# Optimization experiments

Measured on AMD Instinct MI355X. Metric: run time of the kernel, lower is better.

The kernel has to match this reference:

```python
import jax, jax.numpy as jnp
import numpy as np

D_HEAD = 64
KERNEL = 7


def make_neighbourhood_mask(kernel: int, ch: int, cw: int) -> jnp.ndarray:
    """Boolean mask [ch*cw, ch*cw]; True where key is inside the query's k x k window."""
    h_ramp = jnp.arange(ch)
    w_ramp = jnp.arange(cw)
    h_pos, w_pos = jnp.meshgrid(h_ramp, w_ramp, indexing='ij')  # [ch, cw]
    start_h = jnp.clip(h_pos - kernel // 2, 0, ch - kernel)[..., None, None]
    end_h = start_h + kernel
    start_w = jnp.clip(w_pos - kernel // 2, 0, cw - kernel)[..., None, None]
    end_w = start_w + kernel
    h_range = h_ramp.reshape(1, 1, ch, 1)
    w_range = w_ramp.reshape(1, 1, 1, cw)
    mask = (h_range >= start_h) & (h_range < end_h) & (w_range >= start_w) & (w_range < end_w)
    return mask.reshape(ch * cw, ch * cw)


def setup_inputs() -> dict:
    key = jax.random.key(0)
    k1, k2, k3 = jax.random.split(key, 3)
    B, H, W, D = 2, 64, 64, 384
    x = jax.random.normal(k1, (B, H, W, D), dtype=jnp.float32)
    w_qkv = jax.random.normal(k2, (3 * D, D), dtype=jnp.float32) * 0.02
    w_out = jax.random.normal(k3, (D, D), dtype=jnp.float32) * 0.02
    return {"x": x, "w_qkv": w_qkv, "w_out": w_out}


def reference(x, w_qkv, w_out):
    B, H, W, D = x.shape
    nh = D // D_HEAD
    N = H * W
    # qkv projection: Linear(D, 3D, bias=False) -> x @ w_qkv.T
    qkv = jnp.einsum('bhwd,ed->bhwe', x, w_qkv)  # [B,H,W,3D]
    # 'n h w (t nh e) -> t n nh (h w) e'
    qkv = qkv.reshape(B, N, 3, nh, D_HEAD)
    qkv = jnp.transpose(qkv, (2, 0, 3, 1, 4))  # [3, B, nh, N, e]
    q, k, v = qkv[0], qkv[1], qkv[2]
    mask = make_neighbourhood_mask(KERNEL, H, W)  # [N, N] bool
    scale = 1.0 / jnp.sqrt(jnp.asarray(D_HEAD, dtype=x.dtype))
    scores = jnp.einsum('bnqe,bnke->bnqk', q, k) * scale  # [B,nh,N,N]
    neg = jnp.asarray(jnp.finfo(scores.dtype).min, dtype=scores.dtype)
    scores = jnp.where(mask[None, None], scores, neg)
    attn = jax.nn.softmax(scores, axis=-1)
    out = jnp.einsum('bnqk,bnke->bnqe', attn, v)  # [B,nh,N,e]
    # 'n nh (h w) e -> n h w (nh e)'
    out = jnp.transpose(out, (0, 2, 1, 3)).reshape(B, H, W, D)
    return jnp.einsum('bhwd,ed->bhwe', out, w_out)
```

## Files before the change

### kernel.cpp

```cpp
#include <hip/hip_runtime.h>
#include <hip/hip_bf16.h>

typedef __attribute__((ext_vector_type(8))) short bf16x8;
typedef __attribute__((ext_vector_type(4))) short s16x4;
typedef __attribute__((ext_vector_type(4))) float fx4;

#define MFMA16(a, b, c) __builtin_amdgcn_mfma_f32_16x16x32_bf16((a), (b), (c), 0, 0, 0)

__device__ __forceinline__ short f2bf(float f) {
  unsigned u = __float_as_uint(f);
  u += 0x7fffu + ((u >> 16) & 1u);
  return (short)(u >> 16);
}

__device__ __forceinline__ void gl_lds16(const short* g, short* l) {
  __builtin_amdgcn_global_load_lds((const __attribute__((address_space(1))) void*)(g),
                                   (__attribute__((address_space(3))) void*)(l), 16, 0, 0);
}

__global__ __launch_bounds__(256) void convert_k(
    const float* __restrict__ x, const float* __restrict__ wq, const float* __restrict__ wo,
    short* __restrict__ xb, short* __restrict__ wb, short* __restrict__ wob) {
  const int i4 = (blockIdx.x * 256 + threadIdx.x) * 4;
  {
    float4 v = *(const float4*)(x + i4);
    s16x4 s; s[0] = f2bf(v.x); s[1] = f2bf(v.y); s[2] = f2bf(v.z); s[3] = f2bf(v.w);
    *(s16x4*)(xb + i4) = s;
  }
  if (i4 < 1152 * 384) {
    float4 v = *(const float4*)(wq + i4);
    s16x4 s; s[0] = f2bf(v.x); s[1] = f2bf(v.y); s[2] = f2bf(v.z); s[3] = f2bf(v.w);
    *(s16x4*)(wb + i4) = s;
  }
  if (i4 < 384 * 384) {
    float4 v = *(const float4*)(wo + i4);
    s16x4 s; s[0] = f2bf(v.x); s[1] = f2bf(v.y); s[2] = f2bf(v.z); s[3] = f2bf(v.w);
    *(s16x4*)(wob + i4) = s;
  }
}

__global__ __launch_bounds__(256) void qkv_gemm(
    const short* __restrict__ A, const short* __restrict__ Bw,
    short* __restrict__ qb, short* __restrict__ kb, short* __restrict__ vb) {
  __shared__ __align__(16) short As[128 * 64];
  __shared__ __align__(16) short Bs[128 * 64];
  const int orig = (blockIdx.x & 7) * 72 + (blockIdx.x >> 3);
  const int mt = orig / 9, nt = orig % 9;
  const int m0 = mt * 128, n0 = nt * 128;
  const int tid = threadIdx.x;
  const int lane = tid & 63, w = tid >> 6;
  const int wr = w >> 1, wc = w & 1;
  const int l15 = lane & 15, l4 = lane >> 4;
  const int srow = lane >> 3;
  const int scol = ((lane & 7) ^ (srow & 7)) * 8;
  const fx4 vzero = {0.f, 0.f, 0.f, 0.f};
  fx4 acc[4][4];
#pragma unroll
  for (int i = 0; i < 4; i++)
#pragma unroll
    for (int j = 0; j < 4; j++) acc[i][j] = vzero;

  for (int kt = 0; kt < 384; kt += 64) {
    __syncthreads();
#pragma unroll
    for (int q = 0; q < 4; q++) {
      gl_lds16(A  + (size_t)(m0 + w * 32 + q * 8 + srow) * 384 + kt + scol, As + (w * 32 + q * 8) * 64);
      gl_lds16(Bw + (size_t)(n0 + w * 32 + q * 8 + srow) * 384 + kt + scol, Bs + (w * 32 + q * 8) * 64);
    }
    __syncthreads();
    bf16x8 af[4][2], bfr[4][2];
#pragma unroll
    for (int i = 0; i < 4; i++) {
      const int ra = wr * 64 + i * 16 + l15;
      const int rb = wc * 64 + i * 16 + l15;
#pragma unroll
      for (int kk = 0; kk < 2; kk++) {
        af[i][kk]  = *(const bf16x8*)(As + ra * 64 + (((kk * 4 + l4) ^ (ra & 7)) * 8));
        bfr[i][kk] = *(const bf16x8*)(Bs + rb * 64 + (((kk * 4 + l4) ^ (rb & 7)) * 8));
      }
    }
#pragma unroll
    for (int i = 0; i < 4; i++)
#pragma unroll
      for (int j = 0; j < 4; j++) {
        acc[i][j] = MFMA16(af[i][0], bfr[j][0], acc[i][j]);
        acc[i][j] = MFMA16(af[i][1], bfr[j][1], acc[i][j]);
      }
  }
#pragma unroll
  for (int j = 0; j < 4; j++) {
    const int e = n0 + wc * 64 + j * 16 + l15;
    const int t = e / 384;
    const int rem = e - t * 384;
    const int head = rem >> 6, d = rem & 63;
    short* __restrict__ dst = (t == 0) ? qb : (t == 1) ? kb : vb;
#pragma unroll
    for (int i = 0; i < 4; i++) {
      const int mb = m0 + wr * 64 + i * 16 + l4 * 4;
#pragma unroll
      for (int r = 0; r < 4; r++) {
        const int m = mb + r;
        const int b = m >> 12, pix = m & 4095;
        dst[((b * 6 + head) * 4096 + pix) * 64 + d] = f2bf(acc[i][j][r]);
      }
    }
  }
}

__global__ __launch_bounds__(256) void natt_k(
    const short* __restrict__ qg, const short* __restrict__ kg, const short* __restrict__ vg,
    short* __restrict__ ob) {
  __shared__ __align__(16) short lds[30976];
  short* Ks = lds;
  short* Vt = lds + 16128;
  short* Ps = lds;

  const int bid = (blockIdx.x & 7) * 96 + (blockIdx.x >> 3);
  const int tile = bid & 63, bh = bid >> 6;
  const int h0 = (tile >> 3) * 8, w0 = (tile & 7) * 8;
  const int ph0 = max(h0 - 3, 0), pw0 = max(w0 - 3, 0);
  const int prows = min(h0 + 4, 57) + 7 - ph0;
  const int pcols = min(w0 + 4, 57) + 7 - pw0;
  const short* kb = kg + (size_t)bh * 4096 * 64;
  const short* vb = vg + (size_t)bh * 4096 * 64;
  const short* qb = qg + (size_t)bh * 4096 * 64;
  const int tid = threadIdx.x;

  for (int i = tid; i < 224 * 8; i += 256) {
    const int kk = i >> 3, dc = i & 7;
    const int kr = kk >> 4, kc = kk & 15;
    const int krc = min(kr, prows - 1), kcc = min(kc, pcols - 1);
    const int pix = (ph0 + krc) * 64 + (pw0 + kcc);
    *(bf16x8*)(Ks + kk * 72 + dc * 8) = *(const bf16x8*)(kb + pix * 64 + dc * 8);
  }
  if (tid < 224) {
    const int kk = tid;
    const int kr = kk >> 4, kc = kk & 15;
    const int krc = min(kr, prows - 1), kcc = min(kc, pcols - 1);
    const int pix = (ph0 + krc) * 64 + (pw0 + kcc);
#pragma unroll
    for (int dc = 0; dc < 8; dc++) {
      const bf16x8 vv = *(const bf16x8*)(vb + pix * 64 + dc * 8);
#pragma unroll
      for (int j = 0; j < 8; j++) Vt[(dc * 8 + j) * 232 + kk] = vv[j];
    }
  }
  __syncthreads();

  const int lane = tid & 63, w = tid >> 6;
  const int l15 = lane & 15, l4 = lane >> 4;

  const int qa = w * 16 + l15;
  const int qpixa = (h0 + (qa >> 3)) * 64 + (w0 + (qa & 7));
  const bf16x8 aq0 = *(const bf16x8*)(qb + qpixa * 64 + l4 * 8);
  const bf16x8 aq1 = *(const bf16x8*)(qb + qpixa * 64 + 32 + l4 * 8);

  const fx4 vzero = {0.f, 0.f, 0.f, 0.f};
  fx4 s[14];
#pragma unroll
  for (int n = 0; n < 14; n++) s[n] = vzero;
#pragma unroll
  for (int n = 0; n < 14; n++) {
    const bf16x8 b0 = *(const bf16x8*)(Ks + (n * 16 + l15) * 72 + l4 * 8);
    const bf16x8 b1 = *(const bf16x8*)(Ks + (n * 16 + l15) * 72 + 32 + l4 * 8);
    s[n] = MFMA16(aq0, b0, s[n]);
    s[n] = MFMA16(aq1, b1, s[n]);
  }

#pragma unroll
  for (int r = 0; r < 4; r++) {
    const int q = w * 16 + l4 * 4 + r;
    const int qh = h0 + (q >> 3), qw = w0 + (q & 7);
    const int sh = min(max(qh - 3, 0), 57) - ph0;
    const int sw = min(max(qw - 3, 0), 57) - pw0;
    float m = -1e30f;
#pragma unroll
    for (int n = 0; n < 14; n++) {
      const bool valid = (n >= sh) && (n < sh + 7) && (l15 >= sw) && (l15 < sw + 7);
      const float val = valid ? s[n][r] * 0.125f : -1e30f;
      s[n][r] = val;
      m = fmaxf(m, val);
    }
    m = fmaxf(m, __shfl_xor(m, 1));
    m = fmaxf(m, __shfl_xor(m, 2));
    m = fmaxf(m, __shfl_xor(m, 4));
    m = fmaxf(m, __shfl_xor(m, 8));
    float sum = 0.f;
#pragma unroll
    for (int n = 0; n < 14; n++) {
      const float e = __expf(s[n][r] - m);
      s[n][r] = e;
      sum += e;
    }
    sum += __shfl_xor(sum, 1);
    sum += __shfl_xor(sum, 2);
    sum += __shfl_xor(sum, 4);
    sum += __shfl_xor(sum, 8);
    const float inv = 1.f / sum;
#pragma unroll
    for (int n = 0; n < 14; n++) s[n][r] *= inv;
  }

  __syncthreads();

#pragma unroll
  for (int n = 0; n < 14; n++)
#pragma unroll
    for (int r = 0; r < 4; r++)
      Ps[(w * 16 + l4 * 4 + r) * 232 + n * 16 + l15] = f2bf(s[n][r]);

  __syncthreads();

  fx4 o[4];
#pragma unroll
  for (int j = 0; j < 4; j++) o[j] = vzero;
#pragma unroll
  for (int ks = 0; ks < 7; ks++) {
    const bf16x8 pa = *(const bf16x8*)(Ps + (w * 16 + l15) * 232 + ks * 32 + l4 * 8);
#pragma unroll
    for (int j = 0; j < 4; j++) {
      const bf16x8 vf = *(const bf16x8*)(Vt + (j * 16 + l15) * 232 + ks * 32 + l4 * 8);
      o[j] = MFMA16(pa, vf, o[j]);
    }
  }

  const int b = bh / 6, head = bh % 6;
#pragma unroll
  for (int j = 0; j < 4; j++) {
    const int d = j * 16 + l15;
#pragma unroll
    for (int r = 0; r < 4; r++) {
      const int q = w * 16 + l4 * 4 + r;
      const int pix = (h0 + (q >> 3)) * 64 + (w0 + (q & 7));
      ob[(size_t)(b * 4096 + pix) * 384 + head * 64 + d] = f2bf(o[j][r]);
    }
  }
}

__global__ __launch_bounds__(256) void out_gemm(
    const short* __restrict__ A, const short* __restrict__ Bw, float* __restrict__ out) {
  __shared__ __align__(16) short As[64 * 64];
  __shared__ __align__(16) short Bs[128 * 64];
  const int orig = (blockIdx.x & 7) * 48 + (blockIdx.x >> 3);
  const int mt = orig / 3, nt = orig % 3;
  const int m0 = mt * 64, n0 = nt * 128;
  const int tid = threadIdx.x;
  const int lane = tid & 63, w = tid >> 6;
  const int wr = w >> 1, wc = w & 1;
  const int l15 = lane & 15, l4 = lane >> 4;
  const int srow = lane >> 3;
  const int scol = ((lane & 7) ^ (srow & 7)) * 8;
  const fx4 vzero = {0.f, 0.f, 0.f, 0.f};
  fx4 acc[2][4];
#pragma unroll
  for (int i = 0; i < 2; i++)
#pragma unroll
    for (int j = 0; j < 4; j++) acc[i][j] = vzero;

  for (int kt = 0; kt < 384; kt += 64) {
    __syncthreads();
#pragma unroll
    for (int q = 0; q < 2; q++)
      gl_lds16(A + (size_t)(m0 + w * 16 + q * 8 + srow) * 384 + kt + scol, As + (w * 16 + q * 8) * 64);
#pragma unroll
    for (int q = 0; q < 4; q++)
      gl_lds16(Bw + (size_t)(n0 + w * 32 + q * 8 + srow) * 384 + kt + scol, Bs + (w * 32 + q * 8) * 64);
    __syncthreads();
    bf16x8 af[2][2], bfr[4][2];
#pragma unroll
    for (int i = 0; i < 2; i++) {
      const int ra = wr * 32 + i * 16 + l15;
#pragma unroll
      for (int kk = 0; kk < 2; kk++)
        af[i][kk] = *(const bf16x8*)(As + ra * 64 + (((kk * 4 + l4) ^ (ra & 7)) * 8));
    }
#pragma unroll
    for (int j = 0; j < 4; j++) {
      const int rb = wc * 64 + j * 16 + l15;
#pragma unroll
      for (int kk = 0; kk < 2; kk++)
        bfr[j][kk] = *(const bf16x8*)(Bs + rb * 64 + (((kk * 4 + l4) ^ (rb & 7)) * 8));
    }
#pragma unroll
    for (int i = 0; i < 2; i++)
#pragma unroll
      for (int j = 0; j < 4; j++) {
        acc[i][j] = MFMA16(af[i][0], bfr[j][0], acc[i][j]);
        acc[i][j] = MFMA16(af[i][1], bfr[j][1], acc[i][j]);
      }
  }
#pragma unroll
  for (int j = 0; j < 4; j++) {
    const int e = n0 + wc * 64 + j * 16 + l15;
#pragma unroll
    for (int i = 0; i < 2; i++) {
      const int mb = m0 + wr * 32 + i * 16 + l4 * 4;
#pragma unroll
      for (int r = 0; r < 4; r++)
        out[(size_t)(mb + r) * 384 + e] = acc[i][j][r];
    }
  }
}

extern "C" void kernel_launch(void* const* d_in, const int* in_sizes, int n_in,
                              void* d_out, int out_size, void* d_ws, size_t ws_size,
                              hipStream_t stream) {
  const float* x  = (const float*)d_in[0];
  const float* wq = (const float*)d_in[1];
  const float* wo = (const float*)d_in[2];
  float* out = (float*)d_out;

  short* xb  = (short*)d_ws;
  short* wb  = xb + 8192 * 384;
  short* wob = wb + 1152 * 384;
  short* qb  = wob + 384 * 384;
  short* kb  = qb + 3145728;
  short* vb  = kb + 3145728;
  short* ob  = vb + 3145728;

  convert_k<<<3072, 256, 0, stream>>>(x, wq, wo, xb, wb, wob);
  qkv_gemm<<<576, 256, 0, stream>>>(xb, wb, qb, kb, vb);
  natt_k<<<768, 256, 0, stream>>>(qb, kb, vb, ob);
  out_gemm<<<384, 256, 0, stream>>>(ob, wob, out);
}
```

Baseline: 51.62 us.

## Fuse fp32-to-bf16 conversion into GEMM loads with register-prefetched double-buffered LDS

Drops the separate conversion kernel. The QKV and output GEMMs now read fp32 inputs and weights directly, convert them to bf16 in registers, and write them into swizzled LDS. Staging is double-buffered, with the next K-tile prefetched into registers while the current tile runs on MFMA, and one barrier per iteration instead of two. This removes a kernel launch and a full round trip of the bf16 copies through memory. In exchange, fp32 global traffic doubles inside the GEMMs, the weights are converted again by every block, and register pressure and LDS use rise.

```diff
diff --git a/kernel.cpp b/kernel.cpp
--- a/kernel.cpp
+++ b/kernel.cpp
@@ -2,7 +2,6 @@
 #include <hip/hip_bf16.h>
 
 typedef __attribute__((ext_vector_type(8))) short bf16x8;
-typedef __attribute__((ext_vector_type(4))) short s16x4;
 typedef __attribute__((ext_vector_type(4))) float fx4;
 
 #define MFMA16(a, b, c) __builtin_amdgcn_mfma_f32_16x16x32_bf16((a), (b), (c), 0, 0, 0)
@@ -13,37 +12,18 @@
   return (short)(u >> 16);
 }
 
-__device__ __forceinline__ void gl_lds16(const short* g, short* l) {
-  __builtin_amdgcn_global_load_lds((const __attribute__((address_space(1))) void*)(g),
-                                   (__attribute__((address_space(3))) void*)(l), 16, 0, 0);
-}
-
-__global__ __launch_bounds__(256) void convert_k(
-    const float* __restrict__ x, const float* __restrict__ wq, const float* __restrict__ wo,
-    short* __restrict__ xb, short* __restrict__ wb, short* __restrict__ wob) {
-  const int i4 = (blockIdx.x * 256 + threadIdx.x) * 4;
-  {
-    float4 v = *(const float4*)(x + i4);
-    s16x4 s; s[0] = f2bf(v.x); s[1] = f2bf(v.y); s[2] = f2bf(v.z); s[3] = f2bf(v.w);
-    *(s16x4*)(xb + i4) = s;
-  }
-  if (i4 < 1152 * 384) {
-    float4 v = *(const float4*)(wq + i4);
-    s16x4 s; s[0] = f2bf(v.x); s[1] = f2bf(v.y); s[2] = f2bf(v.z); s[3] = f2bf(v.w);
-    *(s16x4*)(wb + i4) = s;
-  }
-  if (i4 < 384 * 384) {
-    float4 v = *(const float4*)(wo + i4);
-    s16x4 s; s[0] = f2bf(v.x); s[1] = f2bf(v.y); s[2] = f2bf(v.z); s[3] = f2bf(v.w);
-    *(s16x4*)(wob + i4) = s;
-  }
+__device__ __forceinline__ bf16x8 cvt8(float4 a, float4 b) {
+  bf16x8 r;
+  r[0] = f2bf(a.x); r[1] = f2bf(a.y); r[2] = f2bf(a.z); r[3] = f2bf(a.w);
+  r[4] = f2bf(b.x); r[5] = f2bf(b.y); r[6] = f2bf(b.z); r[7] = f2bf(b.w);
+  return r;
 }
 
 __global__ __launch_bounds__(256) void qkv_gemm(
-    const short* __restrict__ A, const short* __restrict__ Bw,
+    const float* __restrict__ A, const float* __restrict__ Bw,
     short* __restrict__ qb, short* __restrict__ kb, short* __restrict__ vb) {
-  __shared__ __align__(16) short As[128 * 64];
-  __shared__ __align__(16) short Bs[128 * 64];
+  __shared__ __align__(16) short As[2][128 * 64];
+  __shared__ __align__(16) short Bs[2][128 * 64];
   const int orig = (blockIdx.x & 7) * 72 + (blockIdx.x >> 3);
   const int mt = orig / 9, nt = orig % 9;
   const int m0 = mt * 128, n0 = nt * 128;
@@ -51,8 +31,12 @@
   const int lane = tid & 63, w = tid >> 6;
   const int wr = w >> 1, wc = w & 1;
   const int l15 = lane & 15, l4 = lane >> 4;
-  const int srow = lane >> 3;
-  const int scol = ((lane & 7) ^ (srow & 7)) * 8;
+  const int srow = tid >> 1, shalf = tid & 1;
+  const float* ga = A  + (size_t)(m0 + srow) * 384 + shalf * 32;
+  const float* gb = Bw + (size_t)(n0 + srow) * 384 + shalf * 32;
+  const int wbase = srow * 64;
+  const int sw7 = srow & 7;
+
   const fx4 vzero = {0.f, 0.f, 0.f, 0.f};
   fx4 acc[4][4];
 #pragma unroll
@@ -60,23 +44,39 @@
 #pragma unroll
     for (int j = 0; j < 4; j++) acc[i][j] = vzero;
 
-  for (int kt = 0; kt < 384; kt += 64) {
+  float4 ra[8], rb[8];
+#pragma unroll
+  for (int i = 0; i < 8; i++) {
+    ra[i] = *(const float4*)(ga + i * 4);
+    rb[i] = *(const float4*)(gb + i * 4);
+  }
+#pragma unroll
+  for (int c = 0; c < 4; c++) {
+    *(bf16x8*)(&As[0][wbase + (((shalf * 4 + c) ^ sw7) * 8)]) = cvt8(ra[2 * c], ra[2 * c + 1]);
+    *(bf16x8*)(&Bs[0][wbase + (((shalf * 4 + c) ^ sw7) * 8)]) = cvt8(rb[2 * c], rb[2 * c + 1]);
+  }
+
+  int cur = 0;
+  for (int t = 0; t < 6; ++t) {
+    if (t < 5) {
+#pragma unroll
+      for (int i = 0; i < 8; i++) {
+        ra[i] = *(const float4*)(ga + (t + 1) * 64 + i * 4);
+        rb[i] = *(const float4*)(gb + (t + 1) * 64 + i * 4);
+      }
+    }
     __syncthreads();
-#pragma unroll
-    for (int q = 0; q < 4; q++) {
-      gl_lds16(A  + (size_t)(m0 + w * 32 + q * 8 + srow) * 384 + kt + scol, As + (w * 32 + q * 8) * 64);
-      gl_lds16(Bw + (size_t)(n0 + w * 32 + q * 8 + srow) * 384 + kt + scol, Bs + (w * 32 + q * 8) * 64);
-    }
-    __syncthreads();
+    const short* as_c = As[cur];
+    const short* bs_c = Bs[cur];
     bf16x8 af[4][2], bfr[4][2];
 #pragma unroll
     for (int i = 0; i < 4; i++) {
-      const int ra = wr * 64 + i * 16 + l15;
-      const int rb = wc * 64 + i * 16 + l15;
+      const int ra_ = wr * 64 + i * 16 + l15;
+      const int rb_ = wc * 64 + i * 16 + l15;
 #pragma unroll
       for (int kk = 0; kk < 2; kk++) {
-        af[i][kk]  = *(const bf16x8*)(As + ra * 64 + (((kk * 4 + l4) ^ (ra & 7)) * 8));
-        bfr[i][kk] = *(const bf16x8*)(Bs + rb * 64 + (((kk * 4 + l4) ^ (rb & 7)) * 8));
+        af[i][kk]  = *(const bf16x8*)(as_c + ra_ * 64 + (((kk * 4 + l4) ^ (ra_ & 7)) * 8));
+        bfr[i][kk] = *(const bf16x8*)(bs_c + rb_ * 64 + (((kk * 4 + l4) ^ (rb_ & 7)) * 8));
       }
     }
 #pragma unroll
@@ -86,6 +86,16 @@
         acc[i][j] = MFMA16(af[i][0], bfr[j][0], acc[i][j]);
         acc[i][j] = MFMA16(af[i][1], bfr[j][1], acc[i][j]);
       }
+    if (t < 5) {
+      short* as_n = (short*)As[cur ^ 1];
+      short* bs_n = (short*)Bs[cur ^ 1];
+#pragma unroll
+      for (int c = 0; c < 4; c++) {
+        *(bf16x8*)(&as_n[wbase + (((shalf * 4 + c) ^ sw7) * 8)]) = cvt8(ra[2 * c], ra[2 * c + 1]);
+        *(bf16x8*)(&bs_n[wbase + (((shalf * 4 + c) ^ sw7) * 8)]) = cvt8(rb[2 * c], rb[2 * c + 1]);
+      }
+    }
+    cur ^= 1;
   }
 #pragma unroll
   for (int j = 0; j < 4; j++) {
@@ -238,9 +248,9 @@
 }
 
 __global__ __launch_bounds__(256) void out_gemm(
-    const short* __restrict__ A, const short* __restrict__ Bw, float* __restrict__ out) {
-  __shared__ __align__(16) short As[64 * 64];
-  __shared__ __align__(16) short Bs[128 * 64];
+    const short* __restrict__ A, const float* __restrict__ Bw, float* __restrict__ out) {
+  __shared__ __align__(16) short As[2][64 * 64];
+  __shared__ __align__(16) short Bs[2][128 * 64];
   const int orig = (blockIdx.x & 7) * 48 + (blockIdx.x >> 3);
   const int mt = orig / 3, nt = orig % 3;
   const int m0 = mt * 64, n0 = nt * 128;
@@ -248,8 +258,12 @@
   const int lane = tid & 63, w = tid >> 6;
   const int wr = w >> 1, wc = w & 1;
   const int l15 = lane & 15, l4 = lane >> 4;
-  const int srow = lane >> 3;
-  const int scol = ((lane & 7) ^ (srow & 7)) * 8;
+  const int arow = tid >> 2, aq = tid & 3;
+  const int brow = tid >> 1, bhalf = tid & 1;
+  const short* ga = A  + (size_t)(m0 + arow) * 384 + aq * 16;
+  const float* gb = Bw + (size_t)(n0 + brow) * 384 + bhalf * 32;
+  const int aw7 = arow & 7, bw7 = brow & 7;
+
   const fx4 vzero = {0.f, 0.f, 0.f, 0.f};
   fx4 acc[2][4];
 #pragma unroll
@@ -257,29 +271,44 @@
 #pragma unroll
     for (int j = 0; j < 4; j++) acc[i][j] = vzero;
 
-  for (int kt = 0; kt < 384; kt += 64) {
+  bf16x8 raa[2];
+  float4 rb[8];
+#pragma unroll
+  for (int i = 0; i < 2; i++) raa[i] = *(const bf16x8*)(ga + i * 8);
+#pragma unroll
+  for (int i = 0; i < 8; i++) rb[i] = *(const float4*)(gb + i * 4);
+#pragma unroll
+  for (int c = 0; c < 2; c++)
+    *(bf16x8*)(&As[0][arow * 64 + (((aq * 2 + c) ^ aw7) * 8)]) = raa[c];
+#pragma unroll
+  for (int c = 0; c < 4; c++)
+    *(bf16x8*)(&Bs[0][brow * 64 + (((bhalf * 4 + c) ^ bw7) * 8)]) = cvt8(rb[2 * c], rb[2 * c + 1]);
+
+  int cur = 0;
+  for (int t = 0; t < 6; ++t) {
+    if (t < 5) {
+#pragma unroll
+      for (int i = 0; i < 2; i++) raa[i] = *(const bf16x8*)(ga + (t + 1) * 64 + i * 8);
+#pragma unroll
+      for (int i = 0; i < 8; i++) rb[i] = *(const float4*)(gb + (t + 1) * 64 + i * 4);
+    }
     __syncthreads();
-#pragma unroll
-    for (int q = 0; q < 2; q++)
-      gl_lds16(A + (size_t)(m0 + w * 16 + q * 8 + srow) * 384 + kt + scol, As + (w * 16 + q * 8) * 64);
-#pragma unroll
-    for (int q = 0; q < 4; q++)
-      gl_lds16(Bw + (size_t)(n0 + w * 32 + q * 8 + srow) * 384 + kt + scol, Bs + (w * 32 + q * 8) * 64);
-    __syncthreads();
+    const short* as_c = As[cur];
+    const short* bs_c = Bs[cur];
     bf16x8 af[2][2], bfr[4][2];
 #pragma unroll
     for (int i = 0; i < 2; i++) {
-      const int ra = wr * 32 + i * 16 + l15;
+      const int ra_ = wr * 32 + i * 16 + l15;
 #pragma unroll
       for (int kk = 0; kk < 2; kk++)
-        af[i][kk] = *(const bf16x8*)(As + ra * 64 + (((kk * 4 + l4) ^ (ra & 7)) * 8));
+        af[i][kk] = *(const bf16x8*)(as_c + ra_ * 64 + (((kk * 4 + l4) ^ (ra_ & 7)) * 8));
     }
 #pragma unroll
     for (int j = 0; j < 4; j++) {
-      const int rb = wc * 64 + j * 16 + l15;
+      const int rb_ = wc * 64 + j * 16 + l15;
 #pragma unroll
       for (int kk = 0; kk < 2; kk++)
-        bfr[j][kk] = *(const bf16x8*)(Bs + rb * 64 + (((kk * 4 + l4) ^ (rb & 7)) * 8));
+        bfr[j][kk] = *(const bf16x8*)(bs_c + rb_ * 64 + (((kk * 4 + l4) ^ (rb_ & 7)) * 8));
     }
 #pragma unroll
     for (int i = 0; i < 2; i++)
@@ -288,6 +317,17 @@
         acc[i][j] = MFMA16(af[i][0], bfr[j][0], acc[i][j]);
         acc[i][j] = MFMA16(af[i][1], bfr[j][1], acc[i][j]);
       }
+    if (t < 5) {
+      short* as_n = (short*)As[cur ^ 1];
+      short* bs_n = (short*)Bs[cur ^ 1];
+#pragma unroll
+      for (int c = 0; c < 2; c++)
+        *(bf16x8*)(&as_n[arow * 64 + (((aq * 2 + c) ^ aw7) * 8)]) = raa[c];
+#pragma unroll
+      for (int c = 0; c < 4; c++)
+        *(bf16x8*)(&bs_n[brow * 64 + (((bhalf * 4 + c) ^ bw7) * 8)]) = cvt8(rb[2 * c], rb[2 * c + 1]);
+    }
+    cur ^= 1;
   }
 #pragma unroll
   for (int j = 0; j < 4; j++) {
@@ -310,16 +350,12 @@
   const float* wo = (const float*)d_in[2];
   float* out = (float*)d_out;
 
-  short* xb  = (short*)d_ws;
-  short* wb  = xb + 8192 * 384;
-  short* wob = wb + 1152 * 384;
-  short* qb  = wob + 384 * 384;
-  short* kb  = qb + 3145728;
-  short* vb  = kb + 3145728;
-  short* ob  = vb + 3145728;
-
-  convert_k<<<3072, 256, 0, stream>>>(x, wq, wo, xb, wb, wob);
-  qkv_gemm<<<576, 256, 0, stream>>>(xb, wb, qb, kb, vb);
+  short* qb = (short*)d_ws;
+  short* kb = qb + 3145728;
+  short* vb = kb + 3145728;
+  short* ob = vb + 3145728;
+
+  qkv_gemm<<<576, 256, 0, stream>>>(x, wq, qb, kb, vb);
   natt_k<<<768, 256, 0, stream>>>(qb, kb, vb, ob);
-  out_gemm<<<384, 256, 0, stream>>>(ob, wob, out);
-}
+  out_gemm<<<384, 256, 0, stream>>>(ob, wo, out);
+}
```

New measurement: 80.47 us. 55.9% more time.

## Write V transposed from QKV GEMM so attention loads it with vector copies

Applied to the files above, without the earlier changes.

The QKV projection epilogue now stores V in a [b,head,d,pix] transposed layout using 4-wide vector stores. The attention kernel can then fill its transposed V tile in LDS with contiguous 8-byte copies instead of scalar scatter writes. The window's column start is rounded down to an even value to keep those loads aligned. The trade-off is a strided, less coalesced store pattern in the GEMM epilogue, and column clamping at the right edge is now skipped for V rows, so reads past the window may hit padding columns or the next image row.

```diff
diff --git a/kernel.cpp b/kernel.cpp
--- a/kernel.cpp
+++ b/kernel.cpp
@@ -93,22 +93,27 @@
     const int t = e / 384;
     const int rem = e - t * 384;
     const int head = rem >> 6, d = rem & 63;
-    short* __restrict__ dst = (t == 0) ? qb : (t == 1) ? kb : vb;
 #pragma unroll
     for (int i = 0; i < 4; i++) {
       const int mb = m0 + wr * 64 + i * 16 + l4 * 4;
-#pragma unroll
-      for (int r = 0; r < 4; r++) {
-        const int m = mb + r;
-        const int b = m >> 12, pix = m & 4095;
-        dst[((b * 6 + head) * 4096 + pix) * 64 + d] = f2bf(acc[i][j][r]);
+      const int b = mb >> 12, pix = mb & 4095;
+      if (t == 2) {
+        s16x4 s4;
+#pragma unroll
+        for (int r = 0; r < 4; r++) s4[r] = f2bf(acc[i][j][r]);
+        *(s16x4*)(vb + ((size_t)(b * 6 + head) * 64 + d) * 4096 + pix) = s4;
+      } else {
+        short* __restrict__ dst = (t == 0) ? qb : kb;
+#pragma unroll
+        for (int r = 0; r < 4; r++)
+          dst[((size_t)(b * 6 + head) * 4096 + pix + r) * 64 + d] = f2bf(acc[i][j][r]);
       }
     }
   }
 }
 
 __global__ __launch_bounds__(256) void natt_k(
-    const short* __restrict__ qg, const short* __restrict__ kg, const short* __restrict__ vg,
+    const short* __restrict__ qg, const short* __restrict__ kg, const short* __restrict__ vtg,
     short* __restrict__ ob) {
   __shared__ __align__(16) short lds[30976];
   short* Ks = lds;
@@ -118,12 +123,13 @@
   const int bid = (blockIdx.x & 7) * 96 + (blockIdx.x >> 3);
   const int tile = bid & 63, bh = bid >> 6;
   const int h0 = (tile >> 3) * 8, w0 = (tile & 7) * 8;
-  const int ph0 = max(h0 - 3, 0), pw0 = max(w0 - 3, 0);
+  const int ph0 = max(h0 - 3, 0);
+  const int pw0 = max(w0 - 3, 0) & ~1;
   const int prows = min(h0 + 4, 57) + 7 - ph0;
   const int pcols = min(w0 + 4, 57) + 7 - pw0;
-  const short* kb = kg + (size_t)bh * 4096 * 64;
-  const short* vb = vg + (size_t)bh * 4096 * 64;
-  const short* qb = qg + (size_t)bh * 4096 * 64;
+  const short* kb  = kg  + (size_t)bh * 4096 * 64;
+  const short* vtb = vtg + (size_t)bh * 4096 * 64;
+  const short* qb  = qg  + (size_t)bh * 4096 * 64;
   const int tid = threadIdx.x;
 
   for (int i = tid; i < 224 * 8; i += 256) {
@@ -133,16 +139,15 @@
     const int pix = (ph0 + krc) * 64 + (pw0 + kcc);
     *(bf16x8*)(Ks + kk * 72 + dc * 8) = *(const bf16x8*)(kb + pix * 64 + dc * 8);
   }
-  if (tid < 224) {
-    const int kk = tid;
-    const int kr = kk >> 4, kc = kk & 15;
-    const int krc = min(kr, prows - 1), kcc = min(kc, pcols - 1);
-    const int pix = (ph0 + krc) * 64 + (pw0 + kcc);
-#pragma unroll
-    for (int dc = 0; dc < 8; dc++) {
-      const bf16x8 vv = *(const bf16x8*)(vb + pix * 64 + dc * 8);
-#pragma unroll
-      for (int j = 0; j < 8; j++) Vt[(dc * 8 + j) * 232 + kk] = vv[j];
+  {
+    const int d = tid >> 2, sub = tid & 3;
+    const short* vrow = vtb + (size_t)d * 4096;
+    for (int seg = sub; seg < 14; seg += 4) {
+      const int krc = min(seg, prows - 1);
+      const int src = (ph0 + krc) * 64 + pw0;
+#pragma unroll
+      for (int c = 0; c < 4; c++)
+        *(s16x4*)(Vt + d * 232 + seg * 16 + c * 4) = *(const s16x4*)(vrow + src + c * 4);
     }
   }
   __syncthreads();
```

Result: no change. 51.37 us (-0.5%).
